# Performance work log

Measured on AMD Instinct MI355X. Metric: run time of the kernel, lower is better.

Reference implementation:

```python
import jax, jax.numpy as jnp
import numpy as np

D_MODEL = 512
N_HEADS = 8
D_HEAD = D_MODEL // N_HEADS
EPS = 1e-5


def layer_norm(x, g, b):
    mu = jnp.mean(x, axis=-1, keepdims=True)
    var = jnp.mean(jnp.square(x - mu), axis=-1, keepdims=True)
    return (x - mu) * jax.lax.rsqrt(var + EPS) * g + b


def setup_inputs() -> dict:
    key = jax.random.key(0)
    ks = jax.random.split(key, 8)
    B, L, D = 2, 4096, D_MODEL
    x = jax.random.normal(ks[0], (B, L, D), dtype=jnp.float32)
    # monotonically increasing event timestamps (hours)
    timestamps = jnp.sort(jax.random.uniform(ks[1], (B, L), dtype=jnp.float32) * 1000.0, axis=-1)
    mask = jnp.ones((B, L), dtype=jnp.float32)
    s = 0.02
    return {
        "x": x,
        "timestamps": timestamps,
        "mask": mask,
        "ln1_g": jnp.ones((D,), jnp.float32),
        "ln1_b": jnp.zeros((D,), jnp.float32),
        "w_qkv": jax.random.normal(ks[2], (3 * D, D), jnp.float32) * s,
        "w_out": jax.random.normal(ks[3], (D, D), jnp.float32) * s,
        "decay_rate": jnp.ones((N_HEADS,), jnp.float32) * 0.01,
        "ln2_g": jnp.ones((D,), jnp.float32),
        "ln2_b": jnp.zeros((D,), jnp.float32),
        "w_ff1": jax.random.normal(ks[4], (4 * D, D), jnp.float32) * s,
        "w_ff2": jax.random.normal(ks[5], (D, 4 * D), jnp.float32) * s,
    }


def reference(x, timestamps, mask, ln1_g, ln1_b, w_qkv, w_out, decay_rate, ln2_g, ln2_b, w_ff1, w_ff2):
    B, L, D = x.shape
    H, dh = N_HEADS, D_HEAD
    scale = dh ** (-0.5)

    xn = layer_norm(x, ln1_g, ln1_b)
    qkv = (xn @ w_qkv.T).reshape(B, L, 3, H, dh).transpose(2, 0, 3, 1, 4)  # [3,B,H,L,dh]
    q, k, v = qkv[0], qkv[1], qkv[2]

    attn = jnp.einsum("bhid,bhjd->bhij", q, k) * scale  # [B,H,L,L]

    # temporal-decay bias
    t_diff = jnp.abs(timestamps[:, None, :, None] - timestamps[:, None, None, :]) / 24.0  # [B,1,L,L]
    decay = jax.nn.softplus(decay_rate)[None, :, None, None]  # [1,H,1,1]
    attn = attn - decay * t_diff

    # causal mask
    causal = jnp.triu(jnp.ones((L, L), dtype=bool), k=1)
    attn = jnp.where(causal[None, None], -jnp.inf, attn)

    # padding mask over keys
    pad = (mask == 0)[:, None, None, :]  # [B,1,1,L]
    attn = jnp.where(pad, -jnp.inf, attn)

    attn = jax.nn.softmax(attn, axis=-1)
    out = jnp.einsum("bhij,bhjd->bhid", attn, v).transpose(0, 2, 1, 3).reshape(B, L, D)

    x = x + out @ w_out.T
    h = layer_norm(x, ln2_g, ln2_b)
    x = x + jax.nn.silu(h @ w_ff1.T) @ w_ff2.T
    return x
```

## Files before the change

kernel.cpp:

```cpp
#include <hip/hip_runtime.h>
#include <hip/hip_bf16.h>
#include <cmath>


#define L_SEQ 4096
#define D_MODEL 512
#define N_HEADS 8
#define D_HEAD 64
#define QKV_LD 1536

typedef __attribute__((ext_vector_type(8))) short bf16x8;
typedef __attribute__((ext_vector_type(4))) float f32x4;
typedef __attribute__((ext_vector_type(4))) unsigned u32x4;

__device__ __forceinline__ __hip_bfloat16 f2bf(float v) { return __float2bfloat16(v); }

__device__ __forceinline__ void gl_lds16(const __hip_bfloat16* g, __hip_bfloat16* l) {
  __builtin_amdgcn_global_load_lds((__attribute__((address_space(1))) void*)g,
                                   (__attribute__((address_space(3))) void*)l, 16, 0, 0);
}

__global__ __launch_bounds__(256) void cvt4_kernel(const float* __restrict__ s0, __hip_bfloat16* __restrict__ d0,
                                                   const float* __restrict__ s1, __hip_bfloat16* __restrict__ d1,
                                                   const float* __restrict__ s2, __hip_bfloat16* __restrict__ d2,
                                                   const float* __restrict__ s3, __hip_bfloat16* __restrict__ d3) {
  const int i = blockIdx.x * 256 + threadIdx.x;
  const float* s;
  __hip_bfloat16* d;
  int off;
  if (i < 196608) { s = s0; d = d0; off = i; }
  else if (i < 262144) { s = s1; d = d1; off = i - 196608; }
  else if (i < 524288) { s = s2; d = d2; off = i - 262144; }
  else { s = s3; d = d3; off = i - 524288; }
  const float4 v = ((const float4*)s)[off];
  d[4 * off + 0] = f2bf(v.x);
  d[4 * off + 1] = f2bf(v.y);
  d[4 * off + 2] = f2bf(v.z);
  d[4 * off + 3] = f2bf(v.w);
}

__global__ __launch_bounds__(256) void bias_kernel(const float* __restrict__ ts,
                                                   const float* __restrict__ mask,
                                                   const float* __restrict__ decay_rate,
                                                   float* __restrict__ biasH) {
  const int idx = blockIdx.x * 256 + threadIdx.x;
  const int col = idx & 4095;
  const int h = (idx >> 12) & 7;
  const int b = idx >> 15;
  const float LOG2E = 1.4426950408889634f;
  const float dfac = log1pf(expf(decay_rate[h])) * (1.0f / 24.0f) * LOG2E;
  const float m = mask[b * 4096 + col];
  biasH[idx] = dfac * ts[b * 4096 + col] + (m != 0.f ? 0.f : -1e30f);
}

__global__ __launch_bounds__(256) void ln_kernel(const float* __restrict__ x,
                                                 const float* __restrict__ g,
                                                 const float* __restrict__ b,
                                                 __hip_bfloat16* __restrict__ out) {
  const int row = blockIdx.x;
  const int t = threadIdx.x;
  const float* xr = x + (size_t)row * D_MODEL;
  float v0 = xr[t];
  float v1 = xr[t + 256];
  float s = v0 + v1;
  float qq = v0 * v0 + v1 * v1;
  for (int off = 32; off > 0; off >>= 1) {
    s += __shfl_xor(s, off);
    qq += __shfl_xor(qq, off);
  }
  __shared__ float red[8];
  const int wid = t >> 6;
  if ((t & 63) == 0) { red[wid] = s; red[4 + wid] = qq; }
  __syncthreads();
  s = red[0] + red[1] + red[2] + red[3];
  qq = red[4] + red[5] + red[6] + red[7];
  const float mu = s * (1.0f / 512.0f);
  const float var = fmaxf(qq * (1.0f / 512.0f) - mu * mu, 0.0f);
  const float rstd = rsqrtf(var + 1e-5f);
  __hip_bfloat16* orow = out + (size_t)row * D_MODEL;
  orow[t] = f2bf((v0 - mu) * rstd * g[t] + b[t]);
  orow[t + 256] = f2bf((v1 - mu) * rstd * g[t + 256] + b[t + 256]);
}

__global__ __launch_bounds__(256) void vtrans_kernel(const __hip_bfloat16* __restrict__ qkv,
                                                     __hip_bfloat16* __restrict__ vt) {
  const int gid = blockIdx.x * 256 + threadIdx.x;
  const int l = gid & 4095;
  const int bg = gid >> 12;
  const int b = bg >> 6, g = bg & 63;
  const int h = g >> 3, dg = (g & 7) * 8;
  const __hip_bfloat16* src = qkv + (size_t)(b * L_SEQ + l) * QKV_LD + 1024 + h * 64 + dg;
  bf16x8 v = *(const bf16x8*)src;
  const int kin = l & 63;
  const int sl = (kin & 0x23) | ((kin & 0x10) >> 2) | ((kin & 0x0c) << 1);
  const size_t dbase = (size_t)((b * 8 + h) * 64 + dg) * L_SEQ + (l & ~63) + sl;
  for (int j = 0; j < 8; j++)
    vt[dbase + (size_t)j * L_SEQ] = ((const __hip_bfloat16*)&v)[j];
}

template <int EPI>
__global__ __launch_bounds__(256) void gemm_kernel(const __hip_bfloat16* __restrict__ A,
                                                   const __hip_bfloat16* __restrict__ B,
                                                   int M, int N, int K,
                                                   const float* __restrict__ aux,
                                                   void* __restrict__ C) {
  __shared__ __align__(16) __hip_bfloat16 As[2][128 * 32];
  __shared__ __align__(16) __hip_bfloat16 Bs[2][128 * 32];
  const int tid = threadIdx.x;
  const int lane = tid & 63, w = tid >> 6;
  const int m0 = blockIdx.y * 128, n0 = blockIdx.x * 128;
  const int wm = (w >> 1) * 64, wn = (w & 1) * 64;
  const int r = lane & 15, q = lane >> 4;

  f32x4 acc[4][4];
  const f32x4 zz = {0.f, 0.f, 0.f, 0.f};
  for (int i = 0; i < 4; i++)
    for (int j = 0; j < 4; j++) acc[i][j] = zz;

  const int c0 = tid, c1 = 256 + tid;
  const int row0 = c0 >> 2, kb0 = (c0 & 3) * 8;
  const int row1 = c1 >> 2, kb1 = (c1 & 3) * 8;

#define GEMM_STAGE(k0, buf)                                                     \
  do {                                                                          \
    gl_lds16(A + (size_t)(m0 + row0) * K + ((k0) + kb0), &As[buf][c0 * 8]);     \
    gl_lds16(B + (size_t)(n0 + row0) * K + ((k0) + kb0), &Bs[buf][c0 * 8]);     \
    gl_lds16(A + (size_t)(m0 + row1) * K + ((k0) + kb1), &As[buf][c1 * 8]);     \
    gl_lds16(B + (size_t)(n0 + row1) * K + ((k0) + kb1), &Bs[buf][c1 * 8]);     \
  } while (0)

  GEMM_STAGE(0, 0);
  const int niter = K >> 5;
  for (int it = 0; it < niter; it++) {
    const int cur = it & 1;
    if (it + 1 < niter) {
      GEMM_STAGE((it + 1) << 5, cur ^ 1);
      asm volatile("s_waitcnt vmcnt(4)" ::: "memory");
    } else {
      asm volatile("s_waitcnt vmcnt(0)" ::: "memory");
    }
    __builtin_amdgcn_s_barrier();
    bf16x8 af[4], bfr[4];
    for (int mi = 0; mi < 4; mi++)
      af[mi] = *(const bf16x8*)(&As[cur][(wm + mi * 16 + r) * 32 + q * 8]);
    for (int ni = 0; ni < 4; ni++)
      bfr[ni] = *(const bf16x8*)(&Bs[cur][(wn + ni * 16 + r) * 32 + q * 8]);
    for (int mi = 0; mi < 4; mi++)
      for (int ni = 0; ni < 4; ni++)
        acc[mi][ni] = __builtin_amdgcn_mfma_f32_16x16x32_bf16(af[mi], bfr[ni], acc[mi][ni], 0, 0, 0);
    __builtin_amdgcn_s_barrier();
  }
#undef GEMM_STAGE

  for (int mi = 0; mi < 4; mi++)
    for (int ni = 0; ni < 4; ni++)
      for (int j = 0; j < 4; j++) {
        const int gm = m0 + wm + mi * 16 + q * 4 + j;
        const int gn = n0 + wn + ni * 16 + r;
        float v = acc[mi][ni][j];
        const size_t idx = (size_t)gm * N + gn;
        if (EPI == 0) {
          ((__hip_bfloat16*)C)[idx] = f2bf(v);
        } else {
          v = v / (1.0f + expf(-v));
          ((__hip_bfloat16*)C)[idx] = f2bf(v);
        }
      }
}

__global__ __launch_bounds__(256) void gemm_res64_kernel(const __hip_bfloat16* __restrict__ A,
                                                         const __hip_bfloat16* __restrict__ B,
                                                         int M, int N, int K,
                                                         const float* __restrict__ aux,
                                                         float* __restrict__ C) {
  __shared__ __align__(16) __hip_bfloat16 As[2][64 * 32];
  __shared__ __align__(16) __hip_bfloat16 Bs[2][128 * 32];
  const int tid = threadIdx.x;
  const int lane = tid & 63, w = tid >> 6;
  const int m0 = blockIdx.y * 64, n0 = blockIdx.x * 128;
  const int wm = (w >> 1) * 32, wn = (w & 1) * 64;
  const int r = lane & 15, q = lane >> 4;

  f32x4 acc[2][4];
  const f32x4 zz = {0.f, 0.f, 0.f, 0.f};
  for (int i = 0; i < 2; i++)
    for (int j = 0; j < 4; j++) acc[i][j] = zz;

  const int rowA = tid >> 2, kbA = (tid & 3) * 8;
  const int c0 = tid, c1 = 256 + tid;
  const int rowB0 = c0 >> 2, kb0 = (c0 & 3) * 8;
  const int rowB1 = c1 >> 2, kb1 = (c1 & 3) * 8;

#define GEMM_STAGE64(k0, buf)                                                    \
  do {                                                                           \
    gl_lds16(A + (size_t)(m0 + rowA) * K + ((k0) + kbA), &As[buf][tid * 8]);     \
    gl_lds16(B + (size_t)(n0 + rowB0) * K + ((k0) + kb0), &Bs[buf][c0 * 8]);     \
    gl_lds16(B + (size_t)(n0 + rowB1) * K + ((k0) + kb1), &Bs[buf][c1 * 8]);     \
  } while (0)

  GEMM_STAGE64(0, 0);
  const int niter = K >> 5;
  for (int it = 0; it < niter; it++) {
    const int cur = it & 1;
    if (it + 1 < niter) {
      GEMM_STAGE64((it + 1) << 5, cur ^ 1);
      asm volatile("s_waitcnt vmcnt(3)" ::: "memory");
    } else {
      asm volatile("s_waitcnt vmcnt(0)" ::: "memory");
    }
    __builtin_amdgcn_s_barrier();
    bf16x8 af[2], bfr[4];
    for (int mi = 0; mi < 2; mi++)
      af[mi] = *(const bf16x8*)(&As[cur][(wm + mi * 16 + r) * 32 + q * 8]);
    for (int ni = 0; ni < 4; ni++)
      bfr[ni] = *(const bf16x8*)(&Bs[cur][(wn + ni * 16 + r) * 32 + q * 8]);
    for (int mi = 0; mi < 2; mi++)
      for (int ni = 0; ni < 4; ni++)
        acc[mi][ni] = __builtin_amdgcn_mfma_f32_16x16x32_bf16(af[mi], bfr[ni], acc[mi][ni], 0, 0, 0);
    __builtin_amdgcn_s_barrier();
  }
#undef GEMM_STAGE64

  for (int mi = 0; mi < 2; mi++)
    for (int ni = 0; ni < 4; ni++)
      for (int j = 0; j < 4; j++) {
        const int gm = m0 + wm + mi * 16 + q * 4 + j;
        const int gn = n0 + wn + ni * 16 + r;
        const size_t idx = (size_t)gm * N + gn;
        C[idx] = acc[mi][ni][j] + aux[idx];
      }
}

__device__ __forceinline__ void stage_kv(int w, int lane, int key0,
                                         const __hip_bfloat16* __restrict__ Kg,
                                         const __hip_bfloat16* __restrict__ Vg,
                                         __hip_bfloat16* Ks, __hip_bfloat16* Vs) {
  const int row_in = lane >> 3;
  const int cs = (lane & 7) ^ row_in;
#pragma unroll
  for (int ii = 0; ii < 2; ii++) {
    const int i = w * 2 + ii;
    const int row = i * 8 + row_in;
    gl_lds16(Kg + (size_t)(key0 + row) * QKV_LD + cs * 8, Ks + i * 512 + lane * 8);
    gl_lds16(Vg + (size_t)row * L_SEQ + key0 + cs * 8, Vs + i * 512 + lane * 8);
  }
}

template <bool CAUSAL>
__device__ __forceinline__ void attn_tile(int key0, int lw0, int r, int q,
                                          const __hip_bfloat16* Ks,
                                          const __hip_bfloat16* Vs,
                                          const float* __restrict__ biasHp,
                                          float scale2,
                                          const bf16x8& qf0, const bf16x8& qf1,
                                          f32x4* o, float& ls) {
  const int r7 = r & 7;
  const f32x4 zz = {0.f, 0.f, 0.f, 0.f};
  f32x4 bias4[4];
#pragma unroll
  for (int hc = 0; hc < 4; hc++)
    bias4[hc] = *(const f32x4*)(biasHp + key0 + hc * 16 + q * 4);
  f32x4 s[4];
  __builtin_amdgcn_s_setprio(1);
#pragma unroll
  for (int hc = 0; hc < 4; hc++) {
    const __hip_bfloat16* kr = Ks + (hc * 16 + r) * 64;
    bf16x8 k0 = *(const bf16x8*)(kr + ((q ^ r7) * 8));
    bf16x8 k1 = *(const bf16x8*)(kr + (((q + 4) ^ r7) * 8));
    f32x4 a = zz;
    a = __builtin_amdgcn_mfma_f32_16x16x32_bf16(k0, qf0, a, 0, 0, 0);
    a = __builtin_amdgcn_mfma_f32_16x16x32_bf16(k1, qf1, a, 0, 0, 0);
    s[hc] = a;
  }
  __builtin_amdgcn_s_setprio(0);
  float p[4][4];
  float sum = 0.f;
#pragma unroll
  for (int hc = 0; hc < 4; hc++)
#pragma unroll
    for (int j = 0; j < 4; j++) {
      const float v = fmaf(s[hc][j], scale2, bias4[hc][j]);
      float pv = exp2f(v);
      if (CAUSAL) pv = (key0 + hc * 16 + q * 4 + j <= lw0 + r) ? pv : 0.f;
      p[hc][j] = pv;
      sum += pv;
    }
  ls += sum;
  bf16x8 pa[2];
#pragma unroll
  for (int kc = 0; kc < 2; kc++) {
    u32x4 pw;
    unsigned w0, w1, w2, w3;
    asm("v_cvt_pk_bf16_f32 %0, %1, %2" : "=v"(w0) : "v"(p[2 * kc][0]), "v"(p[2 * kc][1]));
    asm("v_cvt_pk_bf16_f32 %0, %1, %2" : "=v"(w1) : "v"(p[2 * kc][2]), "v"(p[2 * kc][3]));
    asm("v_cvt_pk_bf16_f32 %0, %1, %2" : "=v"(w2) : "v"(p[2 * kc + 1][0]), "v"(p[2 * kc + 1][1]));
    asm("v_cvt_pk_bf16_f32 %0, %1, %2" : "=v"(w3) : "v"(p[2 * kc + 1][2]), "v"(p[2 * kc + 1][3]));
    pw[0] = w0; pw[1] = w1; pw[2] = w2; pw[3] = w3;
    pa[kc] = *(bf16x8*)&pw;
  }
  __builtin_amdgcn_s_setprio(1);
#pragma unroll
  for (int kc = 0; kc < 2; kc++)
#pragma unroll
    for (int c = 0; c < 4; c++) {
      const __hip_bfloat16* vr = Vs + (c * 16 + r) * 64 + (((kc * 4 + q) ^ r7) * 8);
      bf16x8 vf = *(const bf16x8*)vr;
      o[c] = __builtin_amdgcn_mfma_f32_16x16x32_bf16(pa[kc], vf, o[c], 0, 0, 0);
    }
  __builtin_amdgcn_s_setprio(0);
}

__global__ __launch_bounds__(256, 2) void attn_kernel(const __hip_bfloat16* __restrict__ qkv,
                                                      const __hip_bfloat16* __restrict__ vt,
                                                      const float* __restrict__ biasH,
                                                      __hip_bfloat16* __restrict__ out) {
  const int blk = blockIdx.x;
  const int bh = blk & 15;
  const int pr = blk >> 4;
  const int b = bh >> 3, h = bh & 7;
  const int qiA = pr, qiB = 63 - pr;
  const int l0A = qiA * 64, l0B = qiB * 64;
  const int tid = threadIdx.x, lane = tid & 63, w = tid >> 6;
  const int lw0A = l0A + w * 16, lw0B = l0B + w * 16;
  const int r = lane & 15, q = lane >> 4;

  __shared__ __align__(16) __hip_bfloat16 Ksm[2][64 * 64];
  __shared__ __align__(16) __hip_bfloat16 Vsm[2][64 * 64];

  const float LOG2E = 1.4426950408889634f;
  const float scale2 = 0.125f * LOG2E;

  const __hip_bfloat16* Kg = qkv + (size_t)b * L_SEQ * QKV_LD + 512 + h * 64;
  const __hip_bfloat16* Vg = vt + (size_t)bh * 64 * L_SEQ;
  const float* biasHp = biasH + (size_t)bh * L_SEQ;

  stage_kv(w, lane, 0, Kg, Vg, Ksm[0], Vsm[0]);

  bf16x8 qfA0, qfA1, qfB0, qfB1;
  {
    const __hip_bfloat16* qrA = qkv + (size_t)(b * L_SEQ + lw0A + r) * QKV_LD + h * 64 + q * 8;
    qfA0 = *(const bf16x8*)qrA;
    qfA1 = *(const bf16x8*)(qrA + 32);
    const __hip_bfloat16* qrB = qkv + (size_t)(b * L_SEQ + lw0B + r) * QKV_LD + h * 64 + q * 8;
    qfB0 = *(const bf16x8*)qrB;
    qfB1 = *(const bf16x8*)(qrB + 32);
  }

  const f32x4 zz = {0.f, 0.f, 0.f, 0.f};
  f32x4 o[4];
  for (int c = 0; c < 4; c++) o[c] = zz;
  float ls = 0.f;

  const int ntA = qiA + 1;
  const int ntB = qiB + 1;

  for (int t = 0; t < ntA; t++) {
    const int cur = t & 1;
    const int nxt_key0 = (t + 1 < ntA) ? ((t + 1) << 6) : 0;
    stage_kv(w, lane, nxt_key0, Kg, Vg, Ksm[cur ^ 1], Vsm[cur ^ 1]);
    asm volatile("s_waitcnt vmcnt(4)" ::: "memory");
    __builtin_amdgcn_s_barrier();
    if (t < ntA - 1)
      attn_tile<false>(t << 6, lw0A, r, q, Ksm[cur], Vsm[cur], biasHp, scale2, qfA0, qfA1, o, ls);
    else
      attn_tile<true>(t << 6, lw0A, r, q, Ksm[cur], Vsm[cur], biasHp, scale2, qfA0, qfA1, o, ls);
    __builtin_amdgcn_s_barrier();
  }

  {
    float lt = ls;
    lt += __shfl_xor(lt, 16);
    lt += __shfl_xor(lt, 32);
    const float invr = 1.0f / lt;
    float invj[4];
    for (int j = 0; j < 4; j++) invj[j] = __shfl(invr, q * 4 + j);
    for (int c = 0; c < 4; c++)
      for (int j = 0; j < 4; j++) {
        const int rowg = lw0A + q * 4 + j;
        out[(size_t)(b * L_SEQ + rowg) * D_MODEL + h * 64 + c * 16 + r] = f2bf(o[c][j] * invj[j]);
      }
    for (int c = 0; c < 4; c++) o[c] = zz;
    ls = 0.f;
  }

  for (int t = 0; t < ntB; t++) {
    const int cur = (ntA + t) & 1;
    if (t + 1 < ntB) {
      stage_kv(w, lane, (t + 1) << 6, Kg, Vg, Ksm[cur ^ 1], Vsm[cur ^ 1]);
      asm volatile("s_waitcnt vmcnt(4)" ::: "memory");
    } else {
      asm volatile("s_waitcnt vmcnt(0)" ::: "memory");
    }
    __builtin_amdgcn_s_barrier();
    if (t < ntB - 1)
      attn_tile<false>(t << 6, lw0B, r, q, Ksm[cur], Vsm[cur], biasHp, scale2, qfB0, qfB1, o, ls);
    else
      attn_tile<true>(t << 6, lw0B, r, q, Ksm[cur], Vsm[cur], biasHp, scale2, qfB0, qfB1, o, ls);
    __builtin_amdgcn_s_barrier();
  }

  {
    float lt = ls;
    lt += __shfl_xor(lt, 16);
    lt += __shfl_xor(lt, 32);
    const float invr = 1.0f / lt;
    float invj[4];
    for (int j = 0; j < 4; j++) invj[j] = __shfl(invr, q * 4 + j);
    for (int c = 0; c < 4; c++)
      for (int j = 0; j < 4; j++) {
        const int rowg = lw0B + q * 4 + j;
        out[(size_t)(b * L_SEQ + rowg) * D_MODEL + h * 64 + c * 16 + r] = f2bf(o[c][j] * invj[j]);
      }
  }
}

extern "C" void kernel_launch(void* const* d_in, const int* in_sizes, int n_in,
                              void* d_out, int out_size, void* d_ws, size_t ws_size,
                              hipStream_t stream) {
  const float* x = (const float*)d_in[0];
  const float* ts = (const float*)d_in[1];
  const float* mask = (const float*)d_in[2];
  const float* ln1_g = (const float*)d_in[3];
  const float* ln1_b = (const float*)d_in[4];
  const float* w_qkv = (const float*)d_in[5];
  const float* w_out = (const float*)d_in[6];
  const float* decay = (const float*)d_in[7];
  const float* ln2_g = (const float*)d_in[8];
  const float* ln2_b = (const float*)d_in[9];
  const float* w_ff1 = (const float*)d_in[10];
  const float* w_ff2 = (const float*)d_in[11];

  char* ws = (char*)d_ws;
  __hip_bfloat16* wqkv_b = (__hip_bfloat16*)(ws + 0);
  __hip_bfloat16* wout_b = (__hip_bfloat16*)(ws + 1572864);
  __hip_bfloat16* wff1_b = (__hip_bfloat16*)(ws + 2097152);
  __hip_bfloat16* wff2_b = (__hip_bfloat16*)(ws + 4194304);
  __hip_bfloat16* xn = (__hip_bfloat16*)(ws + 6291456);
  __hip_bfloat16* vt = (__hip_bfloat16*)(ws + 6291456);
  __hip_bfloat16* qkv = (__hip_bfloat16*)(ws + 14680064);
  __hip_bfloat16* attnout = (__hip_bfloat16*)(ws + 39845888);
  __hip_bfloat16* h = attnout;
  __hip_bfloat16* ff1out = (__hip_bfloat16*)(ws + 6291456);
  float* x2 = (float*)(ws + 48234496);
  float* biasH = (float*)(ws + 48234496);
  float* out = (float*)d_out;

  const int M = 2 * L_SEQ;

  cvt4_kernel<<<dim3(3072), dim3(256), 0, stream>>>(w_qkv, wqkv_b, w_out, wout_b,
                                                    w_ff1, wff1_b, w_ff2, wff2_b);
  bias_kernel<<<dim3(256), dim3(256), 0, stream>>>(ts, mask, decay, biasH);

  ln_kernel<<<dim3(M), dim3(256), 0, stream>>>(x, ln1_g, ln1_b, xn);
  gemm_kernel<0><<<dim3(12, 64), dim3(256), 0, stream>>>(xn, wqkv_b, M, 1536, 512, nullptr, qkv);
  vtrans_kernel<<<dim3(2048), dim3(256), 0, stream>>>(qkv, vt);
  attn_kernel<<<dim3(512), dim3(256), 0, stream>>>(qkv, vt, biasH, attnout);
  gemm_res64_kernel<<<dim3(4, 128), dim3(256), 0, stream>>>(attnout, wout_b, M, 512, 512, x, x2);
  ln_kernel<<<dim3(M), dim3(256), 0, stream>>>(x2, ln2_g, ln2_b, h);
  gemm_kernel<2><<<dim3(16, 64), dim3(256), 0, stream>>>(h, wff1_b, M, 2048, 512, nullptr, ff1out);
  gemm_res64_kernel<<<dim3(4, 128), dim3(256), 0, stream>>>(ff1out, wff2_b, M, 512, 2048, x2, out);
}
```

Before: 302.6 us.

## Run paired causal query tiles concurrently in 512-thread attention blocks

The attention kernel now uses 8 waves per block. Four waves handle the early query tile and four handle the mirrored late tile at the same time, sharing each staged K/V tile, where before the two tiles ran one after the other. The per-head bias row is loaded into LDS once, and row sums come from an MFMA against a ones vector instead of shuffle reductions. The bias and weight conversion kernels are merged into one launch to save a launch. The risk is that the early-tile waves sit idle for most iterations while the larger block and extra 16 KB of LDS may lower occupancy.

```diff
diff --git a/kernel.cpp b/kernel.cpp
--- a/kernel.cpp
+++ b/kernel.cpp
@@ -20,37 +20,38 @@
                                    (__attribute__((address_space(3))) void*)l, 16, 0, 0);
 }
 
-__global__ __launch_bounds__(256) void cvt4_kernel(const float* __restrict__ s0, __hip_bfloat16* __restrict__ d0,
-                                                   const float* __restrict__ s1, __hip_bfloat16* __restrict__ d1,
-                                                   const float* __restrict__ s2, __hip_bfloat16* __restrict__ d2,
-                                                   const float* __restrict__ s3, __hip_bfloat16* __restrict__ d3) {
+__global__ __launch_bounds__(256) void cvt4b_kernel(const float* __restrict__ s0, __hip_bfloat16* __restrict__ d0,
+                                                    const float* __restrict__ s1, __hip_bfloat16* __restrict__ d1,
+                                                    const float* __restrict__ s2, __hip_bfloat16* __restrict__ d2,
+                                                    const float* __restrict__ s3, __hip_bfloat16* __restrict__ d3,
+                                                    const float* __restrict__ ts,
+                                                    const float* __restrict__ mask,
+                                                    const float* __restrict__ decay_rate,
+                                                    float* __restrict__ biasH) {
   const int i = blockIdx.x * 256 + threadIdx.x;
-  const float* s;
-  __hip_bfloat16* d;
-  int off;
-  if (i < 196608) { s = s0; d = d0; off = i; }
-  else if (i < 262144) { s = s1; d = d1; off = i - 196608; }
-  else if (i < 524288) { s = s2; d = d2; off = i - 262144; }
-  else { s = s3; d = d3; off = i - 524288; }
-  const float4 v = ((const float4*)s)[off];
-  d[4 * off + 0] = f2bf(v.x);
-  d[4 * off + 1] = f2bf(v.y);
-  d[4 * off + 2] = f2bf(v.z);
-  d[4 * off + 3] = f2bf(v.w);
-}
-
-__global__ __launch_bounds__(256) void bias_kernel(const float* __restrict__ ts,
-                                                   const float* __restrict__ mask,
-                                                   const float* __restrict__ decay_rate,
-                                                   float* __restrict__ biasH) {
-  const int idx = blockIdx.x * 256 + threadIdx.x;
-  const int col = idx & 4095;
-  const int h = (idx >> 12) & 7;
-  const int b = idx >> 15;
-  const float LOG2E = 1.4426950408889634f;
-  const float dfac = log1pf(expf(decay_rate[h])) * (1.0f / 24.0f) * LOG2E;
-  const float m = mask[b * 4096 + col];
-  biasH[idx] = dfac * ts[b * 4096 + col] + (m != 0.f ? 0.f : -1e30f);
+  if (i < 786432) {
+    const float* s;
+    __hip_bfloat16* d;
+    int off;
+    if (i < 196608) { s = s0; d = d0; off = i; }
+    else if (i < 262144) { s = s1; d = d1; off = i - 196608; }
+    else if (i < 524288) { s = s2; d = d2; off = i - 262144; }
+    else { s = s3; d = d3; off = i - 524288; }
+    const float4 v = ((const float4*)s)[off];
+    d[4 * off + 0] = f2bf(v.x);
+    d[4 * off + 1] = f2bf(v.y);
+    d[4 * off + 2] = f2bf(v.z);
+    d[4 * off + 3] = f2bf(v.w);
+  } else {
+    const int idx = i - 786432;
+    const int col = idx & 4095;
+    const int h = (idx >> 12) & 7;
+    const int b = idx >> 15;
+    const float LOG2E = 1.4426950408889634f;
+    const float dfac = log1pf(expf(decay_rate[h])) * (1.0f / 24.0f) * LOG2E;
+    const float m = mask[b * 4096 + col];
+    biasH[idx] = dfac * ts[b * 4096 + col] + (m != 0.f ? 0.f : -1e30f);
+  }
 }
 
 __global__ __launch_bounds__(256) void ln_kernel(const float* __restrict__ x,
@@ -231,35 +232,32 @@
       }
 }
 
-__device__ __forceinline__ void stage_kv(int w, int lane, int key0,
-                                         const __hip_bfloat16* __restrict__ Kg,
-                                         const __hip_bfloat16* __restrict__ Vg,
-                                         __hip_bfloat16* Ks, __hip_bfloat16* Vs) {
+__device__ __forceinline__ void stage_kv8(int w, int lane, int key0,
+                                          const __hip_bfloat16* __restrict__ Kg,
+                                          const __hip_bfloat16* __restrict__ Vg,
+                                          __hip_bfloat16* Ks, __hip_bfloat16* Vs) {
   const int row_in = lane >> 3;
   const int cs = (lane & 7) ^ row_in;
-#pragma unroll
-  for (int ii = 0; ii < 2; ii++) {
-    const int i = w * 2 + ii;
-    const int row = i * 8 + row_in;
-    gl_lds16(Kg + (size_t)(key0 + row) * QKV_LD + cs * 8, Ks + i * 512 + lane * 8);
-    gl_lds16(Vg + (size_t)row * L_SEQ + key0 + cs * 8, Vs + i * 512 + lane * 8);
-  }
+  const int row = w * 8 + row_in;
+  gl_lds16(Kg + (size_t)(key0 + row) * QKV_LD + cs * 8, Ks + w * 512 + lane * 8);
+  gl_lds16(Vg + (size_t)row * L_SEQ + key0 + cs * 8, Vs + w * 512 + lane * 8);
 }
 
 template <bool CAUSAL>
 __device__ __forceinline__ void attn_tile(int key0, int lw0, int r, int q,
                                           const __hip_bfloat16* Ks,
                                           const __hip_bfloat16* Vs,
-                                          const float* __restrict__ biasHp,
+                                          const float* biasLds,
                                           float scale2,
                                           const bf16x8& qf0, const bf16x8& qf1,
-                                          f32x4* o, float& ls) {
+                                          const bf16x8& onesf,
+                                          f32x4* o, f32x4& ls) {
   const int r7 = r & 7;
   const f32x4 zz = {0.f, 0.f, 0.f, 0.f};
   f32x4 bias4[4];
 #pragma unroll
   for (int hc = 0; hc < 4; hc++)
-    bias4[hc] = *(const f32x4*)(biasHp + key0 + hc * 16 + q * 4);
+    bias4[hc] = *(const f32x4*)(biasLds + key0 + hc * 16 + q * 4);
   f32x4 s[4];
   __builtin_amdgcn_s_setprio(1);
 #pragma unroll
@@ -274,7 +272,6 @@
   }
   __builtin_amdgcn_s_setprio(0);
   float p[4][4];
-  float sum = 0.f;
 #pragma unroll
   for (int hc = 0; hc < 4; hc++)
 #pragma unroll
@@ -283,9 +280,7 @@
       float pv = exp2f(v);
       if (CAUSAL) pv = (key0 + hc * 16 + q * 4 + j <= lw0 + r) ? pv : 0.f;
       p[hc][j] = pv;
-      sum += pv;
-    }
-  ls += sum;
+    }
   bf16x8 pa[2];
 #pragma unroll
   for (int kc = 0; kc < 2; kc++) {
@@ -300,17 +295,19 @@
   }
   __builtin_amdgcn_s_setprio(1);
 #pragma unroll
-  for (int kc = 0; kc < 2; kc++)
+  for (int kc = 0; kc < 2; kc++) {
 #pragma unroll
     for (int c = 0; c < 4; c++) {
       const __hip_bfloat16* vr = Vs + (c * 16 + r) * 64 + (((kc * 4 + q) ^ r7) * 8);
       bf16x8 vf = *(const bf16x8*)vr;
       o[c] = __builtin_amdgcn_mfma_f32_16x16x32_bf16(pa[kc], vf, o[c], 0, 0, 0);
     }
+    ls = __builtin_amdgcn_mfma_f32_16x16x32_bf16(pa[kc], onesf, ls, 0, 0, 0);
+  }
   __builtin_amdgcn_s_setprio(0);
 }
 
-__global__ __launch_bounds__(256, 2) void attn_kernel(const __hip_bfloat16* __restrict__ qkv,
+__global__ __launch_bounds__(512, 2) void attn_kernel(const __hip_bfloat16* __restrict__ qkv,
                                                       const __hip_bfloat16* __restrict__ vt,
                                                       const float* __restrict__ biasH,
                                                       __hip_bfloat16* __restrict__ out) {
@@ -318,14 +315,16 @@
   const int bh = blk & 15;
   const int pr = blk >> 4;
   const int b = bh >> 3, h = bh & 7;
-  const int qiA = pr, qiB = 63 - pr;
-  const int l0A = qiA * 64, l0B = qiB * 64;
   const int tid = threadIdx.x, lane = tid & 63, w = tid >> 6;
-  const int lw0A = l0A + w * 16, lw0B = l0B + w * 16;
+  const int grp = w >> 2, wg = w & 3;
+  const int qi = grp ? (63 - pr) : pr;
+  const int l0 = qi * 64;
+  const int lw0 = l0 + wg * 16;
   const int r = lane & 15, q = lane >> 4;
 
   __shared__ __align__(16) __hip_bfloat16 Ksm[2][64 * 64];
   __shared__ __align__(16) __hip_bfloat16 Vsm[2][64 * 64];
+  __shared__ __align__(16) float biasLds[4096];
 
   const float LOG2E = 1.4426950408889634f;
   const float scale2 = 0.125f * LOG2E;
@@ -334,84 +333,60 @@
   const __hip_bfloat16* Vg = vt + (size_t)bh * 64 * L_SEQ;
   const float* biasHp = biasH + (size_t)bh * L_SEQ;
 
-  stage_kv(w, lane, 0, Kg, Vg, Ksm[0], Vsm[0]);
-
-  bf16x8 qfA0, qfA1, qfB0, qfB1;
+  stage_kv8(w, lane, 0, Kg, Vg, Ksm[0], Vsm[0]);
+#pragma unroll
+  for (int ii = 0; ii < 2; ii++) {
+    const int fo = (w * 2 + ii) * 256;
+    gl_lds16((const __hip_bfloat16*)(biasHp + fo + lane * 4),
+             (__hip_bfloat16*)(biasLds + fo + lane * 4));
+  }
+
+  bf16x8 qf0, qf1;
   {
-    const __hip_bfloat16* qrA = qkv + (size_t)(b * L_SEQ + lw0A + r) * QKV_LD + h * 64 + q * 8;
-    qfA0 = *(const bf16x8*)qrA;
-    qfA1 = *(const bf16x8*)(qrA + 32);
-    const __hip_bfloat16* qrB = qkv + (size_t)(b * L_SEQ + lw0B + r) * QKV_LD + h * 64 + q * 8;
-    qfB0 = *(const bf16x8*)qrB;
-    qfB1 = *(const bf16x8*)(qrB + 32);
+    const __hip_bfloat16* qrow = qkv + (size_t)(b * L_SEQ + lw0 + r) * QKV_LD + h * 64 + q * 8;
+    qf0 = *(const bf16x8*)qrow;
+    qf1 = *(const bf16x8*)(qrow + 32);
   }
 
   const f32x4 zz = {0.f, 0.f, 0.f, 0.f};
   f32x4 o[4];
   for (int c = 0; c < 4; c++) o[c] = zz;
-  float ls = 0.f;
-
-  const int ntA = qiA + 1;
-  const int ntB = qiB + 1;
-
-  for (int t = 0; t < ntA; t++) {
+  f32x4 ls = zz;
+
+  bf16x8 onesf;
+  for (int i = 0; i < 8; i++) ((short*)&onesf)[i] = (short)0x3F80;
+
+  const int ntA = pr + 1;
+  const int ntB = 64 - pr;
+  const int nt = grp ? ntB : ntA;
+
+  for (int t = 0; t < ntB; t++) {
     const int cur = t & 1;
-    const int nxt_key0 = (t + 1 < ntA) ? ((t + 1) << 6) : 0;
-    stage_kv(w, lane, nxt_key0, Kg, Vg, Ksm[cur ^ 1], Vsm[cur ^ 1]);
-    asm volatile("s_waitcnt vmcnt(4)" ::: "memory");
-    __builtin_amdgcn_s_barrier();
-    if (t < ntA - 1)
-      attn_tile<false>(t << 6, lw0A, r, q, Ksm[cur], Vsm[cur], biasHp, scale2, qfA0, qfA1, o, ls);
-    else
-      attn_tile<true>(t << 6, lw0A, r, q, Ksm[cur], Vsm[cur], biasHp, scale2, qfA0, qfA1, o, ls);
-    __builtin_amdgcn_s_barrier();
-  }
-
-  {
-    float lt = ls;
-    lt += __shfl_xor(lt, 16);
-    lt += __shfl_xor(lt, 32);
-    const float invr = 1.0f / lt;
-    float invj[4];
-    for (int j = 0; j < 4; j++) invj[j] = __shfl(invr, q * 4 + j);
-    for (int c = 0; c < 4; c++)
-      for (int j = 0; j < 4; j++) {
-        const int rowg = lw0A + q * 4 + j;
-        out[(size_t)(b * L_SEQ + rowg) * D_MODEL + h * 64 + c * 16 + r] = f2bf(o[c][j] * invj[j]);
-      }
-    for (int c = 0; c < 4; c++) o[c] = zz;
-    ls = 0.f;
-  }
-
-  for (int t = 0; t < ntB; t++) {
-    const int cur = (ntA + t) & 1;
     if (t + 1 < ntB) {
-      stage_kv(w, lane, (t + 1) << 6, Kg, Vg, Ksm[cur ^ 1], Vsm[cur ^ 1]);
-      asm volatile("s_waitcnt vmcnt(4)" ::: "memory");
+      stage_kv8(w, lane, (t + 1) << 6, Kg, Vg, Ksm[cur ^ 1], Vsm[cur ^ 1]);
+      asm volatile("s_waitcnt vmcnt(2)" ::: "memory");
     } else {
       asm volatile("s_waitcnt vmcnt(0)" ::: "memory");
     }
     __builtin_amdgcn_s_barrier();
-    if (t < ntB - 1)
-      attn_tile<false>(t << 6, lw0B, r, q, Ksm[cur], Vsm[cur], biasHp, scale2, qfB0, qfB1, o, ls);
-    else
-      attn_tile<true>(t << 6, lw0B, r, q, Ksm[cur], Vsm[cur], biasHp, scale2, qfB0, qfB1, o, ls);
-    __builtin_amdgcn_s_barrier();
-  }
-
-  {
-    float lt = ls;
-    lt += __shfl_xor(lt, 16);
-    lt += __shfl_xor(lt, 32);
-    const float invr = 1.0f / lt;
-    float invj[4];
-    for (int j = 0; j < 4; j++) invj[j] = __shfl(invr, q * 4 + j);
-    for (int c = 0; c < 4; c++)
-      for (int j = 0; j < 4; j++) {
-        const int rowg = lw0B + q * 4 + j;
-        out[(size_t)(b * L_SEQ + rowg) * D_MODEL + h * 64 + c * 16 + r] = f2bf(o[c][j] * invj[j]);
-      }
-  }
+    if (t < nt) {
+      if (t == nt - 1)
+        attn_tile<true>(t << 6, lw0, r, q, Ksm[cur], Vsm[cur], biasLds, scale2, qf0, qf1,
+                        onesf, o, ls);
+      else
+        attn_tile<false>(t << 6, lw0, r, q, Ksm[cur], Vsm[cur], biasLds, scale2, qf0, qf1,
+                         onesf, o, ls);
+    }
+    __builtin_amdgcn_s_barrier();
+  }
+
+  float invj[4];
+  for (int j = 0; j < 4; j++) invj[j] = 1.0f / ls[j];
+  for (int c = 0; c < 4; c++)
+    for (int j = 0; j < 4; j++) {
+      const int rowg = lw0 + q * 4 + j;
+      out[(size_t)(b * L_SEQ + rowg) * D_MODEL + h * 64 + c * 16 + r] = f2bf(o[c][j] * invj[j]);
+    }
 }
 
 extern "C" void kernel_launch(void* const* d_in, const int* in_sizes, int n_in,
@@ -447,14 +422,14 @@
 
   const int M = 2 * L_SEQ;
 
-  cvt4_kernel<<<dim3(3072), dim3(256), 0, stream>>>(w_qkv, wqkv_b, w_out, wout_b,
-                                                    w_ff1, wff1_b, w_ff2, wff2_b);
-  bias_kernel<<<dim3(256), dim3(256), 0, stream>>>(ts, mask, decay, biasH);
+  cvt4b_kernel<<<dim3(3328), dim3(256), 0, stream>>>(w_qkv, wqkv_b, w_out, wout_b,
+                                                     w_ff1, wff1_b, w_ff2, wff2_b,
+                                                     ts, mask, decay, biasH);
 
   ln_kernel<<<dim3(M), dim3(256), 0, stream>>>(x, ln1_g, ln1_b, xn);
   gemm_kernel<0><<<dim3(12, 64), dim3(256), 0, stream>>>(xn, wqkv_b, M, 1536, 512, nullptr, qkv);
   vtrans_kernel<<<dim3(2048), dim3(256), 0, stream>>>(qkv, vt);
-  attn_kernel<<<dim3(512), dim3(256), 0, stream>>>(qkv, vt, biasH, attnout);
+  attn_kernel<<<dim3(512), dim3(512), 0, stream>>>(qkv, vt, biasH, attnout);
   gemm_res64_kernel<<<dim3(4, 128), dim3(256), 0, stream>>>(attnout, wout_b, M, 512, 512, x, x2);
   ln_kernel<<<dim3(M), dim3(256), 0, stream>>>(x2, ln2_g, ln2_b, h);
   gemm_kernel<2><<<dim3(16, 64), dim3(256), 0, stream>>>(h, wff1_b, M, 2048, 512, nullptr, ff1out);
```

New measurement: 293.9 us. -2.9%, faster.
